# Performance work log

Measured on AMD Instinct MI355X. Metric: run time of the kernel, lower is better.

## Reference

```python
import jax, jax.numpy as jnp
import numpy as np

N, E = 50000, 800000
IN_F, HID, NCLS, NLAYERS = 64, 64, 2, 3
BN_EPS = 1e-5


def batch_norm(x, gamma, beta):
    # training-mode BatchNorm1d: biased batch statistics over the node/edge dim
    m = jnp.mean(x, axis=0)
    v = jnp.var(x, axis=0)
    return gamma * (x - m) * jax.lax.rsqrt(v + BN_EPS) + beta


def setup_inputs() -> dict:
    key = jax.random.key(0)
    ks = jax.random.split(key, 24)
    L, Lp1 = NLAYERS, NLAYERS + 1

    def lin(k, fan_in, shape):
        bound = 1.0 / np.sqrt(fan_in)
        return jax.random.uniform(k, shape, jnp.float32, -bound, bound)

    return {
        "h": jax.random.normal(ks[0], (N, IN_F), jnp.float32),
        "src": jax.random.randint(ks[1], (E,), 0, N, jnp.int32),
        "dst": jax.random.randint(ks[2], (E,), 0, N, jnp.int32),
        "emb_W": lin(ks[3], IN_F, (IN_F, HID)),
        "emb_b": lin(ks[4], IN_F, (HID,)),
        "mlp_W1": lin(ks[5], HID, (L, HID, HID)),
        "mlp_b1": lin(ks[6], HID, (L, HID)),
        "mlp_bn_g": jnp.ones((L, HID), jnp.float32),
        "mlp_bn_b": jnp.zeros((L, HID), jnp.float32),
        "mlp_W2": lin(ks[7], HID, (L, HID, HID)),
        "mlp_b2": lin(ks[8], HID, (L, HID)),
        "apply_bn_g": jnp.ones((L, HID), jnp.float32),
        "apply_bn_b": jnp.zeros((L, HID), jnp.float32),
        "out_bn_g": jnp.ones((L, HID), jnp.float32),
        "out_bn_b": jnp.zeros((L, HID), jnp.float32),
        "pred_W1": lin(ks[9], 2 * HID, (Lp1, 2 * HID, HID)),
        "pred_b1": lin(ks[10], 2 * HID, (Lp1, HID)),
        "pred_W2": lin(ks[11], HID, (Lp1, HID, NCLS)),
        "pred_b2": lin(ks[12], HID, (Lp1, NCLS)),
    }


def reference(h, src, dst, emb_W, emb_b, mlp_W1, mlp_b1, mlp_bn_g, mlp_bn_b,
              mlp_W2, mlp_b2, apply_bn_g, apply_bn_b, out_bn_g, out_bn_b,
              pred_W1, pred_b1, pred_W2, pred_b2):
    n_layers = mlp_W1.shape[0]
    n_nodes = h.shape[0]

    def edge_feat(hn):
        # concat src and dst node features per edge -> [E, 2*HID]
        return jnp.concatenate([hn[src], hn[dst]], axis=1)

    hn = h @ emb_W + emb_b  # embedding_h
    edge_reps = [edge_feat(hn)]

    for i in range(n_layers):
        # GINConv (sum aggregation, eps=0): (1+eps)*h_v + sum_{u->v} h_u
        agg = jax.ops.segment_sum(hn[src], dst, num_segments=n_nodes)
        z = hn + agg
        # MLP (depth 2): Linear -> BN -> ReLU -> Linear
        z = jax.nn.relu(batch_norm(z @ mlp_W1[i] + mlp_b1[i], mlp_bn_g[i], mlp_bn_b[i]))
        z = z @ mlp_W2[i] + mlp_b2[i]
        # ApplyNodeFunc: BN + ReLU
        z = jax.nn.relu(batch_norm(z, apply_bn_g[i], apply_bn_b[i]))
        # outer per-layer BN + ReLU
        hn = jax.nn.relu(batch_norm(z, out_bn_g[i], out_bn_b[i]))
        edge_reps.append(edge_feat(hn))

    # sum of per-layer edge predictions: Linear(2h->h) -> ReLU -> Linear(h->ncls)
    score = jnp.zeros((src.shape[0], pred_W2.shape[-1]), h.dtype)
    for i, e in enumerate(edge_reps):
        score = score + jax.nn.relu(e @ pred_W1[i] + pred_b1[i]) @ pred_W2[i] + pred_b2[i]
    return score
```

## Files before the change

### kernel.cpp

```cpp
#include <hip/hip_runtime.h>
#include <hip/hip_bf16.h>


#define BN_EPS 1e-5f

static __device__ __forceinline__ float bf2f(ushort u) {
  return __uint_as_float(((unsigned)u) << 16);
}

__global__ __launch_bounds__(256) void hist_kernel(const int* __restrict__ dst,
                                                   int* __restrict__ deg, int E) {
  int i = blockIdx.x * blockDim.x + threadIdx.x;
  int stride = gridDim.x * blockDim.x;
  for (; i < E; i += stride) atomicAdd(&deg[dst[i]], 1);
}

__global__ __launch_bounds__(256) void scan1_kernel(const int* __restrict__ deg,
                                                    int* __restrict__ rowstart,
                                                    int* __restrict__ partials, int N) {
  __shared__ int wsum[4];
  int tid = threadIdx.x;
  int lane = tid & 63, w = tid >> 6;
  int base = blockIdx.x * 1024 + tid * 4;
  int d0 = 0, d1 = 0, d2 = 0, d3 = 0;
  if (base + 3 < N) {
    int4 v = *reinterpret_cast<const int4*>(deg + base);
    d0 = v.x; d1 = v.y; d2 = v.z; d3 = v.w;
  } else {
    if (base + 0 < N) d0 = deg[base + 0];
    if (base + 1 < N) d1 = deg[base + 1];
    if (base + 2 < N) d2 = deg[base + 2];
  }
  int t0 = d0, t1 = t0 + d1, t2 = t1 + d2, t3 = t2 + d3;
  int tot = t3;
  int inc = tot;
#pragma unroll
  for (int off = 1; off < 64; off <<= 1) {
    int v = __shfl_up(inc, off);
    if (lane >= off) inc += v;
  }
  if (lane == 63) wsum[w] = inc;
  __syncthreads();
  int woff = 0;
  for (int k = 0; k < w; ++k) woff += wsum[k];
  int excl = woff + inc - tot;
  if (base + 0 < N) rowstart[base + 0] = excl;
  if (base + 1 < N) rowstart[base + 1] = excl + t0;
  if (base + 2 < N) rowstart[base + 2] = excl + t1;
  if (base + 3 < N) rowstart[base + 3] = excl + t2;
  if (tid == 255) partials[blockIdx.x] = excl + t3;
}

__global__ __launch_bounds__(256) void scan3_kernel(const int* __restrict__ partials,
                                                    int* __restrict__ rowstart,
                                                    int* __restrict__ cursor,
                                                    int N, int NB, int E) {
  __shared__ int s_off;
  int tid = threadIdx.x;
  if (tid < 64) {
    int v = (tid < NB) ? partials[tid] : 0;
    int inc = v;
#pragma unroll
    for (int off = 1; off < 64; off <<= 1) {
      int t = __shfl_up(inc, off);
      if (tid >= off) inc += t;
    }
    if (tid == (int)blockIdx.x) s_off = inc - v;
  }
  __syncthreads();
  int off = s_off;
  int base = blockIdx.x * 1024 + tid * 4;
#pragma unroll
  for (int k = 0; k < 4; ++k) {
    int i = base + k;
    if (i < N) {
      int r = rowstart[i] + off;
      rowstart[i] = r;
      cursor[i] = r;
    }
  }
  if (blockIdx.x == 0 && tid == 0) rowstart[N] = E;
}

__global__ __launch_bounds__(256) void fill_kernel(const int* __restrict__ src,
                                                   const int* __restrict__ dst,
                                                   int* __restrict__ cursor,
                                                   int2* __restrict__ epack, int E) {
  int i = blockIdx.x * blockDim.x + threadIdx.x;
  int stride = gridDim.x * blockDim.x;
  for (; i < E; i += stride) {
    int p = atomicAdd(&cursor[dst[i]], 1);
    epack[p] = make_int2(src[i], i);
  }
}

template <int TR>
__global__ __launch_bounds__(256) void agg_gemm_kernel(
    const float* __restrict__ c, const ushort* __restrict__ cb,
    const int2* __restrict__ epack, const int* __restrict__ rowstart,
    const float* __restrict__ W, const float* __restrict__ bias,
    const float* __restrict__ stats_tr, const float* __restrict__ g_tr,
    const float* __restrict__ b_tr, float* __restrict__ out,
    float* __restrict__ stats_out, int N) {
  __shared__ float sW[64][64];
  __shared__ float sx[32][64];
  __shared__ float red[2][4][64];
  int tid = threadIdx.x, lane = tid & 63, w = tid >> 6;
  int n0 = blockIdx.x * 32;
#pragma unroll
  for (int r = 0; r < 16; ++r) {
    int idx = r * 256 + tid;
    sW[idx >> 6][idx & 63] = W[idx];
  }
  float sc = 1.f, sh = 0.f;
  if (TR) {
    float invN = 1.0f / (float)N;
    float m = stats_tr[lane] * invN;
    float var = stats_tr[64 + lane] * invN - m * m;
    sc = g_tr[lane] * rsqrtf(var + BN_EPS);
    sh = b_tr[lane] - m * sc;
  }
  for (int j = 0; j < 8; ++j) {
    int v = n0 + w * 8 + j;
    float acc = 0.f;
    if (v < N) {
      float x0 = c[(size_t)v * 64 + lane];
      acc = TR ? fmaxf(x0 * sc + sh, 0.f) : x0;
      int p = rowstart[v], pe = rowstart[v + 1];
      for (; p + 8 <= pe; p += 8) {
        int u[8];
#pragma unroll
        for (int k = 0; k < 8; ++k) u[k] = epack[p + k].x;
        float x[8];
#pragma unroll
        for (int k = 0; k < 8; ++k) x[k] = bf2f(cb[(size_t)u[k] * 64 + lane]);
#pragma unroll
        for (int k = 0; k < 8; ++k) acc += TR ? fmaxf(x[k] * sc + sh, 0.f) : x[k];
      }
      for (; p < pe; ++p) {
        float x = bf2f(cb[(size_t)epack[p].x * 64 + lane]);
        acc += TR ? fmaxf(x * sc + sh, 0.f) : x;
      }
    }
    sx[w * 8 + j][lane] = acc;
  }
  __syncthreads();
  float o[8];
  float bz = bias[lane];
#pragma unroll
  for (int j = 0; j < 8; ++j) o[j] = bz;
  for (int k = 0; k < 64; ++k) {
    float wv = sW[k][lane];
#pragma unroll
    for (int j = 0; j < 8; ++j) o[j] = fmaf(sx[w * 8 + j][k], wv, o[j]);
  }
  float ps = 0.f, pq = 0.f;
#pragma unroll
  for (int j = 0; j < 8; ++j) {
    int n = n0 + w * 8 + j;
    if (n < N) {
      out[(size_t)n * 64 + lane] = o[j];
      ps += o[j];
      pq += o[j] * o[j];
    }
  }
  if (stats_out) {
    red[0][w][lane] = ps;
    red[1][w][lane] = pq;
    __syncthreads();
    if (w == 0) {
      float s = red[0][0][lane] + red[0][1][lane] + red[0][2][lane] + red[0][3][lane];
      float q = red[1][0][lane] + red[1][1][lane] + red[1][2][lane] + red[1][3][lane];
      atomicAdd(&stats_out[lane], s);
      atomicAdd(&stats_out[64 + lane], q);
    }
  }
}

__global__ __launch_bounds__(256) void gemm64_kernel(
    const float* __restrict__ in, const float* __restrict__ W,
    const float* __restrict__ bias, const float* __restrict__ stats_in,
    const float* __restrict__ g_in, const float* __restrict__ b_in,
    float* __restrict__ out, float* __restrict__ stats_out,
    __hip_bfloat16* __restrict__ out_bf, int N) {
  __shared__ float sW[64][64];
  __shared__ float sx[32][64];
  __shared__ float red[2][4][64];
  int tid = threadIdx.x;
  int lane = tid & 63, w = tid >> 6;
  int n0 = blockIdx.x * 32;
#pragma unroll
  for (int r = 0; r < 16; ++r) {
    int idx = r * 256 + tid;
    sW[idx >> 6][idx & 63] = W[idx];
  }
  float sc = 1.f, sh = 0.f;
  if (stats_in) {
    float invN = 1.0f / (float)N;
    float m = stats_in[lane] * invN;
    float var = stats_in[64 + lane] * invN - m * m;
    sc = g_in[lane] * rsqrtf(var + BN_EPS);
    sh = b_in[lane] - m * sc;
  }
#pragma unroll
  for (int r = 0; r < 8; ++r) {
    int idx = r * 256 + tid;
    int n = n0 + (idx >> 6);
    float x = (n < N) ? in[(size_t)n * 64 + lane] : 0.f;
    if (stats_in) x = fmaxf(x * sc + sh, 0.f);
    sx[idx >> 6][lane] = x;
  }
  __syncthreads();
  float acc[8];
  float bz = bias ? bias[lane] : 0.f;
#pragma unroll
  for (int j = 0; j < 8; ++j) acc[j] = bz;
  for (int k = 0; k < 64; ++k) {
    float wv = sW[k][lane];
#pragma unroll
    for (int j = 0; j < 8; ++j) acc[j] = fmaf(sx[w * 8 + j][k], wv, acc[j]);
  }
  float ps = 0.f, pq = 0.f;
#pragma unroll
  for (int j = 0; j < 8; ++j) {
    int n = n0 + w * 8 + j;
    if (n < N) {
      out[(size_t)n * 64 + lane] = acc[j];
      if (out_bf) out_bf[(size_t)n * 64 + lane] = __float2bfloat16(acc[j]);
      ps += acc[j];
      pq += acc[j] * acc[j];
    }
  }
  if (stats_out) {
    red[0][w][lane] = ps;
    red[1][w][lane] = pq;
    __syncthreads();
    if (w == 0) {
      float s = red[0][0][lane] + red[0][1][lane] + red[0][2][lane] + red[0][3][lane];
      float q = red[1][0][lane] + red[1][1][lane] + red[1][2][lane] + red[1][3][lane];
      atomicAdd(&stats_out[lane], s);
      atomicAdd(&stats_out[64 + lane], q);
    }
  }
}

__global__ __launch_bounds__(256) void proj_kernel(
    const float* __restrict__ c, const float* __restrict__ W1,
    const float* __restrict__ b1, const float* __restrict__ stats_in,
    const float* __restrict__ g_in, const float* __restrict__ b_in,
    __hip_bfloat16* __restrict__ P1, __hip_bfloat16* __restrict__ P2, int N) {
  __shared__ float sWa[64][64];
  __shared__ float sWb[64][64];
  __shared__ float sx[32][64];
  int tid = threadIdx.x, lane = tid & 63, w = tid >> 6;
  int n0 = blockIdx.x * 32;
#pragma unroll
  for (int r = 0; r < 16; ++r) {
    int idx = r * 256 + tid;
    sWa[idx >> 6][idx & 63] = W1[idx];
    sWb[idx >> 6][idx & 63] = W1[4096 + idx];
  }
  float sc = 1.f, sh = 0.f;
  if (stats_in) {
    float invN = 1.0f / (float)N;
    float m = stats_in[lane] * invN;
    float var = stats_in[64 + lane] * invN - m * m;
    sc = g_in[lane] * rsqrtf(var + BN_EPS);
    sh = b_in[lane] - m * sc;
  }
#pragma unroll
  for (int r = 0; r < 8; ++r) {
    int idx = r * 256 + tid;
    int n = n0 + (idx >> 6);
    float x = (n < N) ? c[(size_t)n * 64 + lane] : 0.f;
    if (stats_in) x = fmaxf(x * sc + sh, 0.f);
    sx[idx >> 6][lane] = x;
  }
  __syncthreads();
  float a1[8], a2[8];
  float bz = b1[lane];
#pragma unroll
  for (int j = 0; j < 8; ++j) { a1[j] = bz; a2[j] = 0.f; }
  for (int k = 0; k < 64; ++k) {
    float wa = sWa[k][lane];
    float wb = sWb[k][lane];
#pragma unroll
    for (int j = 0; j < 8; ++j) {
      float x = sx[w * 8 + j][k];
      a1[j] = fmaf(x, wa, a1[j]);
      a2[j] = fmaf(x, wb, a2[j]);
    }
  }
#pragma unroll
  for (int j = 0; j < 8; ++j) {
    int n = n0 + w * 8 + j;
    if (n < N) {
      P1[(size_t)n * 64 + lane] = __float2bfloat16(a1[j]);
      P2[(size_t)n * 64 + lane] = __float2bfloat16(a2[j]);
    }
  }
}

__global__ __launch_bounds__(256) void bnrelu_kernel(
    const float* __restrict__ in, const float* __restrict__ stats_in,
    const float* __restrict__ g_in, const float* __restrict__ b_in,
    float* __restrict__ out, float* __restrict__ stats_out,
    __hip_bfloat16* __restrict__ out_bf, int N) {
  __shared__ float red[2][4][64];
  int tid = threadIdx.x;
  int lane = tid & 63, w = tid >> 6;
  float invN = 1.0f / (float)N;
  float m = stats_in[lane] * invN;
  float var = stats_in[64 + lane] * invN - m * m;
  float sc = g_in[lane] * rsqrtf(var + BN_EPS);
  float sh = b_in[lane] - m * sc;
  float ps = 0.f, pq = 0.f;
  int rows_per_grid = gridDim.x * (blockDim.x >> 6);
  for (int n = blockIdx.x * (blockDim.x >> 6) + w; n < N; n += rows_per_grid) {
    float x = fmaxf(in[(size_t)n * 64 + lane] * sc + sh, 0.f);
    out[(size_t)n * 64 + lane] = x;
    if (out_bf) out_bf[(size_t)n * 64 + lane] = __float2bfloat16(x);
    ps += x;
    pq += x * x;
  }
  if (stats_out) {
    red[0][w][lane] = ps;
    red[1][w][lane] = pq;
    __syncthreads();
    if (w == 0) {
      float s = red[0][0][lane] + red[0][1][lane] + red[0][2][lane] + red[0][3][lane];
      float q = red[1][0][lane] + red[1][1][lane] + red[1][2][lane] + red[1][3][lane];
      atomicAdd(&stats_out[lane], s);
      atomicAdd(&stats_out[64 + lane], q);
    }
  }
}

__global__ __launch_bounds__(256) void edge_score_csr_kernel(
    const ushort* __restrict__ P1, const ushort* __restrict__ P2,
    const int* __restrict__ rowstart, const int2* __restrict__ epack,
    const float* __restrict__ W2, const float* __restrict__ b2,
    float2* __restrict__ sc, int N, int first) {
  int lane = threadIdx.x & 63;
  int v = blockIdx.x * 4 + (threadIdx.x >> 6);
  if (v >= N) return;
  int sub = lane & 7;
  int grp = lane >> 3;
  float w[16];
  const float4* wp = reinterpret_cast<const float4*>(W2 + sub * 16);
#pragma unroll
  for (int k = 0; k < 4; ++k) {
    float4 t = wp[k];
    w[4 * k + 0] = t.x; w[4 * k + 1] = t.y; w[4 * k + 2] = t.z; w[4 * k + 3] = t.w;
  }
  float bb0 = b2[0], bb1 = b2[1];
  uint4 pb = *reinterpret_cast<const uint4*>(P2 + (size_t)v * 64 + sub * 8);
  unsigned bv[4] = {pb.x, pb.y, pb.z, pb.w};
  int p0 = rowstart[v], p1 = rowstart[v + 1];
  for (int p = p0 + grp; p < p1; p += 8) {
    int s = epack[p].x;
    uint4 pa = *reinterpret_cast<const uint4*>(P1 + (size_t)s * 64 + sub * 8);
    unsigned av[4] = {pa.x, pa.y, pa.z, pa.w};
    float q0 = 0.f, q1 = 0.f;
#pragma unroll
    for (int k = 0; k < 4; ++k) {
      float a_lo = __uint_as_float(av[k] << 16);
      float a_hi = __uint_as_float(av[k] & 0xffff0000u);
      float b_lo = __uint_as_float(bv[k] << 16);
      float b_hi = __uint_as_float(bv[k] & 0xffff0000u);
      float v0 = fmaxf(a_lo + b_lo, 0.f);
      float v1 = fmaxf(a_hi + b_hi, 0.f);
      q0 = fmaf(v0, w[4 * k + 0], fmaf(v1, w[4 * k + 2], q0));
      q1 = fmaf(v0, w[4 * k + 1], fmaf(v1, w[4 * k + 3], q1));
    }
#pragma unroll
    for (int mm = 1; mm < 8; mm <<= 1) {
      q0 += __shfl_xor(q0, mm);
      q1 += __shfl_xor(q1, mm);
    }
    if (sub == 0) {
      float o0 = q0 + bb0, o1 = q1 + bb1;
      if (!first) {
        float2 prev = sc[p];
        o0 += prev.x;
        o1 += prev.y;
      }
      sc[p] = make_float2(o0, o1);
    }
  }
}

__global__ __launch_bounds__(256) void scatter_kernel(const float2* __restrict__ sc,
                                                      const int2* __restrict__ epack,
                                                      float2* __restrict__ out, int E) {
  int i = blockIdx.x * blockDim.x + threadIdx.x;
  int stride = gridDim.x * blockDim.x;
  for (; i < E; i += stride) out[epack[i].y] = sc[i];
}

extern "C" void kernel_launch(void* const* d_in, const int* in_sizes, int n_in,
                              void* d_out, int out_size, void* d_ws, size_t ws_size,
                              hipStream_t stream) {
  const float* h          = (const float*)d_in[0];
  const int*   src        = (const int*)d_in[1];
  const int*   dst        = (const int*)d_in[2];
  const float* emb_W      = (const float*)d_in[3];
  const float* emb_b      = (const float*)d_in[4];
  const float* mlp_W1     = (const float*)d_in[5];
  const float* mlp_b1     = (const float*)d_in[6];
  const float* mlp_bn_g   = (const float*)d_in[7];
  const float* mlp_bn_b   = (const float*)d_in[8];
  const float* mlp_W2     = (const float*)d_in[9];
  const float* mlp_b2     = (const float*)d_in[10];
  const float* apply_bn_g = (const float*)d_in[11];
  const float* apply_bn_b = (const float*)d_in[12];
  const float* out_bn_g   = (const float*)d_in[13];
  const float* out_bn_b   = (const float*)d_in[14];
  const float* pred_W1    = (const float*)d_in[15];
  const float* pred_b1    = (const float*)d_in[16];
  const float* pred_W2    = (const float*)d_in[17];
  const float* pred_b2    = (const float*)d_in[18];

  const int N = in_sizes[0] / 64;
  const int E = in_sizes[1];
  const size_t NF = (size_t)N * 64;
  const int NB1 = (N + 1023) / 1024;

  float* ws = (float*)d_ws;
  float* c  = ws;
  float* z1 = c + NF;
  float* z2 = z1 + NF;
  __hip_bfloat16* cb = (__hip_bfloat16*)(z2 + NF);
  __hip_bfloat16* P1 = cb + NF;
  __hip_bfloat16* P2 = P1 + NF;
  int2*   epack  = (int2*)(P2 + NF);
  float2* scbuf  = (float2*)(epack + E);
  int* rowstart  = (int*)(scbuf + E);
  int* cursor    = rowstart + (N + 64);
  int* partials  = cursor + (N + 64);
  int* deg       = partials + 64;
  float* stats   = (float*)(deg + (N + 64));

  size_t need = (size_t)((char*)(stats + 9 * 128) - (char*)d_ws);
  if (need > ws_size) return;

  hipMemsetAsync(deg, 0, ((size_t)(N + 64) + 9 * 128) * sizeof(int), stream);

  const int gemmBlocks = (N + 31) / 32;
  const int nodeBlocks = (N + 3) / 4;

  gemm64_kernel<<<gemmBlocks, 256, 0, stream>>>(h, emb_W, emb_b, nullptr, nullptr,
                                                nullptr, c, nullptr, cb, N);
  hist_kernel<<<1024, 256, 0, stream>>>(dst, deg, E);
  scan1_kernel<<<NB1, 256, 0, stream>>>(deg, rowstart, partials, N);
  scan3_kernel<<<NB1, 256, 0, stream>>>(partials, rowstart, cursor, N, NB1, E);
  fill_kernel<<<1024, 256, 0, stream>>>(src, dst, cursor, epack, E);

  proj_kernel<<<gemmBlocks, 256, 0, stream>>>(c, pred_W1, pred_b1, nullptr, nullptr,
                                              nullptr, P1, P2, N);
  edge_score_csr_kernel<<<nodeBlocks, 256, 0, stream>>>(
      (const ushort*)P1, (const ushort*)P2, rowstart, epack, pred_W2, pred_b2,
      scbuf, N, 1);

  for (int i = 0; i < 3; ++i) {
    float* st1 = stats + (size_t)(3 * i + 0) * 128;
    float* st2 = stats + (size_t)(3 * i + 1) * 128;
    float* st3 = stats + (size_t)(3 * i + 2) * 128;
    const float* stP = (i == 0) ? nullptr : stats + (size_t)(3 * (i - 1) + 2) * 128;
    const float* gP  = (i == 0) ? nullptr : out_bn_g + (i - 1) * 64;
    const float* bP  = (i == 0) ? nullptr : out_bn_b + (i - 1) * 64;

    if (i == 0)
      agg_gemm_kernel<0><<<gemmBlocks, 256, 0, stream>>>(
          c, (const ushort*)cb, epack, rowstart, mlp_W1 + (size_t)i * 4096,
          mlp_b1 + i * 64, nullptr, nullptr, nullptr, z1, st1, N);
    else
      agg_gemm_kernel<1><<<gemmBlocks, 256, 0, stream>>>(
          c, (const ushort*)cb, epack, rowstart, mlp_W1 + (size_t)i * 4096,
          mlp_b1 + i * 64, stP, gP, bP, z1, st1, N);
    gemm64_kernel<<<gemmBlocks, 256, 0, stream>>>(z1, mlp_W2 + (size_t)i * 4096,
                                                  mlp_b2 + i * 64, st1,
                                                  mlp_bn_g + i * 64, mlp_bn_b + i * 64,
                                                  z2, st2, nullptr, N);
    bnrelu_kernel<<<784, 256, 0, stream>>>(z2, st2, apply_bn_g + i * 64,
                                           apply_bn_b + i * 64, c, st3, cb, N);
    proj_kernel<<<gemmBlocks, 256, 0, stream>>>(c, pred_W1 + (size_t)(i + 1) * 8192,
                                                pred_b1 + (i + 1) * 64, st3,
                                                out_bn_g + i * 64, out_bn_b + i * 64,
                                                P1, P2, N);
    edge_score_csr_kernel<<<nodeBlocks, 256, 0, stream>>>(
        (const ushort*)P1, (const ushort*)P2, rowstart, epack,
        pred_W2 + (i + 1) * 128, pred_b2 + (i + 1) * 2, scbuf, N, 0);
  }

  scatter_kernel<<<2048, 256, 0, stream>>>(scbuf, epack, (float2*)d_out, E);
}
```

Before: 972.8 us.

## Fuse neighbor aggregation into edge-score kernel via interleaved node feature buffer

Interleaves the bf16 projected source features and the bf16 node features into one 128-wide row per node, so a single 16-byte gather per edge feeds both the edge-score MLP and the GIN sum aggregation. The separate aggregation+GEMM kernel is replaced by a plain GEMM over an aggregated buffer written by the fused score/aggregate kernel. This removes one full CSR gather pass per layer. In exchange, each edge is handled by a 16-lane group (half the lanes idle on each branch), and the 4-way edge split lowers parallelism compared with the 8-way score kernel.

```diff
diff --git a/kernel.cpp b/kernel.cpp
--- a/kernel.cpp
+++ b/kernel.cpp
@@ -4,8 +4,11 @@
 
 #define BN_EPS 1e-5f
 
-static __device__ __forceinline__ float bf2f(ushort u) {
-  return __uint_as_float(((unsigned)u) << 16);
+static __device__ __forceinline__ float bf2f_lo(unsigned u) {
+  return __uint_as_float(u << 16);
+}
+static __device__ __forceinline__ float bf2f_hi(unsigned u) {
+  return __uint_as_float(u & 0xffff0000u);
 }
 
 __global__ __launch_bounds__(256) void hist_kernel(const int* __restrict__ dst,
@@ -94,18 +97,17 @@
   }
 }
 
-template <int TR>
-__global__ __launch_bounds__(256) void agg_gemm_kernel(
-    const float* __restrict__ c, const ushort* __restrict__ cb,
-    const int2* __restrict__ epack, const int* __restrict__ rowstart,
-    const float* __restrict__ W, const float* __restrict__ bias,
-    const float* __restrict__ stats_tr, const float* __restrict__ g_tr,
-    const float* __restrict__ b_tr, float* __restrict__ out,
-    float* __restrict__ stats_out, int N) {
+__global__ __launch_bounds__(256) void gemm64_kernel(
+    const float* __restrict__ in, const float* __restrict__ W,
+    const float* __restrict__ bias, const float* __restrict__ stats_in,
+    const float* __restrict__ g_in, const float* __restrict__ b_in,
+    float* __restrict__ out, float* __restrict__ stats_out,
+    ushort* __restrict__ out_g, int N) {
   __shared__ float sW[64][64];
   __shared__ float sx[32][64];
   __shared__ float red[2][4][64];
-  int tid = threadIdx.x, lane = tid & 63, w = tid >> 6;
+  int tid = threadIdx.x;
+  int lane = tid & 63, w = tid >> 6;
   int n0 = blockIdx.x * 32;
 #pragma unroll
   for (int r = 0; r < 16; ++r) {
@@ -113,55 +115,43 @@
     sW[idx >> 6][idx & 63] = W[idx];
   }
   float sc = 1.f, sh = 0.f;
-  if (TR) {
+  if (stats_in) {
     float invN = 1.0f / (float)N;
-    float m = stats_tr[lane] * invN;
-    float var = stats_tr[64 + lane] * invN - m * m;
-    sc = g_tr[lane] * rsqrtf(var + BN_EPS);
-    sh = b_tr[lane] - m * sc;
-  }
-  for (int j = 0; j < 8; ++j) {
-    int v = n0 + w * 8 + j;
-    float acc = 0.f;
-    if (v < N) {
-      float x0 = c[(size_t)v * 64 + lane];
-      acc = TR ? fmaxf(x0 * sc + sh, 0.f) : x0;
-      int p = rowstart[v], pe = rowstart[v + 1];
-      for (; p + 8 <= pe; p += 8) {
-        int u[8];
-#pragma unroll
-        for (int k = 0; k < 8; ++k) u[k] = epack[p + k].x;
-        float x[8];
-#pragma unroll
-        for (int k = 0; k < 8; ++k) x[k] = bf2f(cb[(size_t)u[k] * 64 + lane]);
-#pragma unroll
-        for (int k = 0; k < 8; ++k) acc += TR ? fmaxf(x[k] * sc + sh, 0.f) : x[k];
-      }
-      for (; p < pe; ++p) {
-        float x = bf2f(cb[(size_t)epack[p].x * 64 + lane]);
-        acc += TR ? fmaxf(x * sc + sh, 0.f) : x;
-      }
-    }
-    sx[w * 8 + j][lane] = acc;
+    float m = stats_in[lane] * invN;
+    float var = stats_in[64 + lane] * invN - m * m;
+    sc = g_in[lane] * rsqrtf(var + BN_EPS);
+    sh = b_in[lane] - m * sc;
+  }
+#pragma unroll
+  for (int r = 0; r < 8; ++r) {
+    int idx = r * 256 + tid;
+    int n = n0 + (idx >> 6);
+    float x = (n < N) ? in[(size_t)n * 64 + lane] : 0.f;
+    if (stats_in) x = fmaxf(x * sc + sh, 0.f);
+    sx[idx >> 6][lane] = x;
   }
   __syncthreads();
-  float o[8];
-  float bz = bias[lane];
-#pragma unroll
-  for (int j = 0; j < 8; ++j) o[j] = bz;
+  float acc[8];
+  float bz = bias ? bias[lane] : 0.f;
+#pragma unroll
+  for (int j = 0; j < 8; ++j) acc[j] = bz;
   for (int k = 0; k < 64; ++k) {
     float wv = sW[k][lane];
 #pragma unroll
-    for (int j = 0; j < 8; ++j) o[j] = fmaf(sx[w * 8 + j][k], wv, o[j]);
+    for (int j = 0; j < 8; ++j) acc[j] = fmaf(sx[w * 8 + j][k], wv, acc[j]);
   }
   float ps = 0.f, pq = 0.f;
 #pragma unroll
   for (int j = 0; j < 8; ++j) {
     int n = n0 + w * 8 + j;
     if (n < N) {
-      out[(size_t)n * 64 + lane] = o[j];
-      ps += o[j];
-      pq += o[j] * o[j];
+      out[(size_t)n * 64 + lane] = acc[j];
+      if (out_g) {
+        __hip_bfloat16 b = __float2bfloat16(acc[j]);
+        out_g[(size_t)n * 128 + lane] = *reinterpret_cast<ushort*>(&b);
+      }
+      ps += acc[j];
+      pq += acc[j] * acc[j];
     }
   }
   if (stats_out) {
@@ -177,22 +167,21 @@
   }
 }
 
-__global__ __launch_bounds__(256) void gemm64_kernel(
-    const float* __restrict__ in, const float* __restrict__ W,
-    const float* __restrict__ bias, const float* __restrict__ stats_in,
+__global__ __launch_bounds__(256) void proj_kernel(
+    const float* __restrict__ c, const float* __restrict__ W1,
+    const float* __restrict__ b1, const float* __restrict__ stats_in,
     const float* __restrict__ g_in, const float* __restrict__ b_in,
-    float* __restrict__ out, float* __restrict__ stats_out,
-    __hip_bfloat16* __restrict__ out_bf, int N) {
-  __shared__ float sW[64][64];
+    ushort* __restrict__ G, ushort* __restrict__ P2, int N) {
+  __shared__ float sWa[64][64];
+  __shared__ float sWb[64][64];
   __shared__ float sx[32][64];
-  __shared__ float red[2][4][64];
-  int tid = threadIdx.x;
-  int lane = tid & 63, w = tid >> 6;
+  int tid = threadIdx.x, lane = tid & 63, w = tid >> 6;
   int n0 = blockIdx.x * 32;
 #pragma unroll
   for (int r = 0; r < 16; ++r) {
     int idx = r * 256 + tid;
-    sW[idx >> 6][idx & 63] = W[idx];
+    sWa[idx >> 6][idx & 63] = W1[idx];
+    sWb[idx >> 6][idx & 63] = W1[4096 + idx];
   }
   float sc = 1.f, sh = 0.f;
   if (stats_in) {
@@ -206,72 +195,6 @@
   for (int r = 0; r < 8; ++r) {
     int idx = r * 256 + tid;
     int n = n0 + (idx >> 6);
-    float x = (n < N) ? in[(size_t)n * 64 + lane] : 0.f;
-    if (stats_in) x = fmaxf(x * sc + sh, 0.f);
-    sx[idx >> 6][lane] = x;
-  }
-  __syncthreads();
-  float acc[8];
-  float bz = bias ? bias[lane] : 0.f;
-#pragma unroll
-  for (int j = 0; j < 8; ++j) acc[j] = bz;
-  for (int k = 0; k < 64; ++k) {
-    float wv = sW[k][lane];
-#pragma unroll
-    for (int j = 0; j < 8; ++j) acc[j] = fmaf(sx[w * 8 + j][k], wv, acc[j]);
-  }
-  float ps = 0.f, pq = 0.f;
-#pragma unroll
-  for (int j = 0; j < 8; ++j) {
-    int n = n0 + w * 8 + j;
-    if (n < N) {
-      out[(size_t)n * 64 + lane] = acc[j];
-      if (out_bf) out_bf[(size_t)n * 64 + lane] = __float2bfloat16(acc[j]);
-      ps += acc[j];
-      pq += acc[j] * acc[j];
-    }
-  }
-  if (stats_out) {
-    red[0][w][lane] = ps;
-    red[1][w][lane] = pq;
-    __syncthreads();
-    if (w == 0) {
-      float s = red[0][0][lane] + red[0][1][lane] + red[0][2][lane] + red[0][3][lane];
-      float q = red[1][0][lane] + red[1][1][lane] + red[1][2][lane] + red[1][3][lane];
-      atomicAdd(&stats_out[lane], s);
-      atomicAdd(&stats_out[64 + lane], q);
-    }
-  }
-}
-
-__global__ __launch_bounds__(256) void proj_kernel(
-    const float* __restrict__ c, const float* __restrict__ W1,
-    const float* __restrict__ b1, const float* __restrict__ stats_in,
-    const float* __restrict__ g_in, const float* __restrict__ b_in,
-    __hip_bfloat16* __restrict__ P1, __hip_bfloat16* __restrict__ P2, int N) {
-  __shared__ float sWa[64][64];
-  __shared__ float sWb[64][64];
-  __shared__ float sx[32][64];
-  int tid = threadIdx.x, lane = tid & 63, w = tid >> 6;
-  int n0 = blockIdx.x * 32;
-#pragma unroll
-  for (int r = 0; r < 16; ++r) {
-    int idx = r * 256 + tid;
-    sWa[idx >> 6][idx & 63] = W1[idx];
-    sWb[idx >> 6][idx & 63] = W1[4096 + idx];
-  }
-  float sc = 1.f, sh = 0.f;
-  if (stats_in) {
-    float invN = 1.0f / (float)N;
-    float m = stats_in[lane] * invN;
-    float var = stats_in[64 + lane] * invN - m * m;
-    sc = g_in[lane] * rsqrtf(var + BN_EPS);
-    sh = b_in[lane] - m * sc;
-  }
-#pragma unroll
-  for (int r = 0; r < 8; ++r) {
-    int idx = r * 256 + tid;
-    int n = n0 + (idx >> 6);
     float x = (n < N) ? c[(size_t)n * 64 + lane] : 0.f;
     if (stats_in) x = fmaxf(x * sc + sh, 0.f);
     sx[idx >> 6][lane] = x;
@@ -295,8 +218,10 @@
   for (int j = 0; j < 8; ++j) {
     int n = n0 + w * 8 + j;
     if (n < N) {
-      P1[(size_t)n * 64 + lane] = __float2bfloat16(a1[j]);
-      P2[(size_t)n * 64 + lane] = __float2bfloat16(a2[j]);
+      __hip_bfloat16 b1v = __float2bfloat16(a1[j]);
+      __hip_bfloat16 b2v = __float2bfloat16(a2[j]);
+      G[(size_t)n * 128 + lane] = *reinterpret_cast<ushort*>(&b1v);
+      P2[(size_t)n * 64 + lane] = *reinterpret_cast<ushort*>(&b2v);
     }
   }
 }
@@ -305,7 +230,7 @@
     const float* __restrict__ in, const float* __restrict__ stats_in,
     const float* __restrict__ g_in, const float* __restrict__ b_in,
     float* __restrict__ out, float* __restrict__ stats_out,
-    __hip_bfloat16* __restrict__ out_bf, int N) {
+    ushort* __restrict__ out_g, int N) {
   __shared__ float red[2][4][64];
   int tid = threadIdx.x;
   int lane = tid & 63, w = tid >> 6;
@@ -319,7 +244,8 @@
   for (int n = blockIdx.x * (blockDim.x >> 6) + w; n < N; n += rows_per_grid) {
     float x = fmaxf(in[(size_t)n * 64 + lane] * sc + sh, 0.f);
     out[(size_t)n * 64 + lane] = x;
-    if (out_bf) out_bf[(size_t)n * 64 + lane] = __float2bfloat16(x);
+    __hip_bfloat16 b = __float2bfloat16(x);
+    out_g[(size_t)n * 128 + lane] = *reinterpret_cast<ushort*>(&b);
     ps += x;
     pq += x * x;
   }
@@ -336,8 +262,115 @@
   }
 }
 
+template <int TR>
+__global__ __launch_bounds__(256) void score_agg_kernel(
+    const ushort* __restrict__ G, const ushort* __restrict__ P2,
+    const float* __restrict__ c, const int* __restrict__ rowstart,
+    const int2* __restrict__ epack, const float* __restrict__ W2,
+    const float* __restrict__ b2, const float* __restrict__ stats_tr,
+    const float* __restrict__ g_tr, const float* __restrict__ b_tr,
+    float2* __restrict__ sc, float* __restrict__ zb, int N, int first) {
+  int lane = threadIdx.x & 63;
+  int v = blockIdx.x * 4 + (threadIdx.x >> 6);
+  if (v >= N) return;
+  int grp = lane >> 4;
+  int g16 = lane & 15;
+  int sub = g16 & 7;
+  float w[16];
+  {
+    const float4* wp = reinterpret_cast<const float4*>(W2 + sub * 16);
+#pragma unroll
+    for (int k = 0; k < 4; ++k) {
+      float4 t = wp[k];
+      w[4 * k + 0] = t.x; w[4 * k + 1] = t.y; w[4 * k + 2] = t.z; w[4 * k + 3] = t.w;
+    }
+  }
+  float bb0 = b2[0], bb1 = b2[1];
+  uint4 pb = *reinterpret_cast<const uint4*>(P2 + (size_t)v * 64 + sub * 8);
+  unsigned bv[4] = {pb.x, pb.y, pb.z, pb.w};
+  float scv[8], shv[8];
+  if (TR) {
+    float invN = 1.0f / (float)N;
+#pragma unroll
+    for (int k = 0; k < 8; ++k) {
+      int f = sub * 8 + k;
+      float m = stats_tr[f] * invN;
+      float var = stats_tr[64 + f] * invN - m * m;
+      scv[k] = g_tr[f] * rsqrtf(var + BN_EPS);
+      shv[k] = b_tr[f] - m * scv[k];
+    }
+  }
+  float acc[8];
+#pragma unroll
+  for (int k = 0; k < 8; ++k) acc[k] = 0.f;
+
+  int p0 = rowstart[v], p1 = rowstart[v + 1];
+  for (int p = p0 + grp; p < p1; p += 4) {
+    int s = epack[p].x;
+    uint4 row = *reinterpret_cast<const uint4*>(G + (size_t)s * 128 + g16 * 8);
+    unsigned rv[4] = {row.x, row.y, row.z, row.w};
+    float q0 = 0.f, q1 = 0.f;
+    if (g16 < 8) {
+#pragma unroll
+      for (int k = 0; k < 4; ++k) {
+        float v0 = fmaxf(bf2f_lo(rv[k]) + bf2f_lo(bv[k]), 0.f);
+        float v1 = fmaxf(bf2f_hi(rv[k]) + bf2f_hi(bv[k]), 0.f);
+        q0 = fmaf(v0, w[4 * k + 0], fmaf(v1, w[4 * k + 2], q0));
+        q1 = fmaf(v0, w[4 * k + 1], fmaf(v1, w[4 * k + 3], q1));
+      }
+    } else {
+#pragma unroll
+      for (int k = 0; k < 4; ++k) {
+        float x0 = bf2f_lo(rv[k]);
+        float x1 = bf2f_hi(rv[k]);
+        if (TR) {
+          x0 = fmaxf(x0 * scv[2 * k] + shv[2 * k], 0.f);
+          x1 = fmaxf(x1 * scv[2 * k + 1] + shv[2 * k + 1], 0.f);
+        }
+        acc[2 * k] += x0;
+        acc[2 * k + 1] += x1;
+      }
+    }
+#pragma unroll
+    for (int mm = 1; mm < 8; mm <<= 1) {
+      q0 += __shfl_xor(q0, mm);
+      q1 += __shfl_xor(q1, mm);
+    }
+    if (g16 == 0) {
+      float o0 = q0 + bb0, o1 = q1 + bb1;
+      if (!first) {
+        float2 prev = sc[p];
+        o0 += prev.x;
+        o1 += prev.y;
+      }
+      sc[p] = make_float2(o0, o1);
+    }
+  }
+#pragma unroll
+  for (int k = 0; k < 8; ++k) {
+    acc[k] += __shfl_xor(acc[k], 16);
+    acc[k] += __shfl_xor(acc[k], 32);
+  }
+  if (grp == 0 && g16 >= 8) {
+    const float* cv = c + (size_t)v * 64 + sub * 8;
+    float4 c0 = *reinterpret_cast<const float4*>(cv);
+    float4 c1 = *reinterpret_cast<const float4*>(cv + 4);
+    float cf[8] = {c0.x, c0.y, c0.z, c0.w, c1.x, c1.y, c1.z, c1.w};
+    float ov[8];
+#pragma unroll
+    for (int k = 0; k < 8; ++k) {
+      float x = cf[k];
+      if (TR) x = fmaxf(x * scv[k] + shv[k], 0.f);
+      ov[k] = acc[k] + x;
+    }
+    float* zp = zb + (size_t)v * 64 + sub * 8;
+    *reinterpret_cast<float4*>(zp) = make_float4(ov[0], ov[1], ov[2], ov[3]);
+    *reinterpret_cast<float4*>(zp + 4) = make_float4(ov[4], ov[5], ov[6], ov[7]);
+  }
+}
+
 __global__ __launch_bounds__(256) void edge_score_csr_kernel(
-    const ushort* __restrict__ P1, const ushort* __restrict__ P2,
+    const ushort* __restrict__ G, const ushort* __restrict__ P2,
     const int* __restrict__ rowstart, const int2* __restrict__ epack,
     const float* __restrict__ W2, const float* __restrict__ b2,
     float2* __restrict__ sc, int N, int first) {
@@ -359,17 +392,13 @@
   int p0 = rowstart[v], p1 = rowstart[v + 1];
   for (int p = p0 + grp; p < p1; p += 8) {
     int s = epack[p].x;
-    uint4 pa = *reinterpret_cast<const uint4*>(P1 + (size_t)s * 64 + sub * 8);
+    uint4 pa = *reinterpret_cast<const uint4*>(G + (size_t)s * 128 + sub * 8);
     unsigned av[4] = {pa.x, pa.y, pa.z, pa.w};
     float q0 = 0.f, q1 = 0.f;
 #pragma unroll
     for (int k = 0; k < 4; ++k) {
-      float a_lo = __uint_as_float(av[k] << 16);
-      float a_hi = __uint_as_float(av[k] & 0xffff0000u);
-      float b_lo = __uint_as_float(bv[k] << 16);
-      float b_hi = __uint_as_float(bv[k] & 0xffff0000u);
-      float v0 = fmaxf(a_lo + b_lo, 0.f);
-      float v1 = fmaxf(a_hi + b_hi, 0.f);
+      float v0 = fmaxf(bf2f_lo(av[k]) + bf2f_lo(bv[k]), 0.f);
+      float v1 = fmaxf(bf2f_hi(av[k]) + bf2f_hi(bv[k]), 0.f);
       q0 = fmaf(v0, w[4 * k + 0], fmaf(v1, w[4 * k + 2], q0));
       q1 = fmaf(v0, w[4 * k + 1], fmaf(v1, w[4 * k + 3], q1));
     }
@@ -427,19 +456,18 @@
   const int NB1 = (N + 1023) / 1024;
 
   float* ws = (float*)d_ws;
-  float* c  = ws;
-  float* z1 = c + NF;
-  float* z2 = z1 + NF;
-  __hip_bfloat16* cb = (__hip_bfloat16*)(z2 + NF);
-  __hip_bfloat16* P1 = cb + NF;
-  __hip_bfloat16* P2 = P1 + NF;
-  int2*   epack  = (int2*)(P2 + NF);
-  float2* scbuf  = (float2*)(epack + E);
-  int* rowstart  = (int*)(scbuf + E);
-  int* cursor    = rowstart + (N + 64);
-  int* partials  = cursor + (N + 64);
-  int* deg       = partials + 64;
-  float* stats   = (float*)(deg + (N + 64));
+  float* c   = ws;
+  float* z1  = c + NF;
+  float* zb  = z1 + NF;
+  ushort* G  = (ushort*)(zb + NF);
+  ushort* P2 = G + (size_t)N * 128;
+  int2*   epack = (int2*)(P2 + NF);
+  float2* scbuf = (float2*)(epack + E);
+  int* rowstart = (int*)(scbuf + E);
+  int* cursor   = rowstart + (N + 64);
+  int* partials = cursor + (N + 64);
+  int* deg      = partials + 64;
+  float* stats  = (float*)(deg + (N + 64));
 
   size_t need = (size_t)((char*)(stats + 9 * 128) - (char*)d_ws);
   if (need > ws_size) return;
@@ -450,47 +478,46 @@
   const int nodeBlocks = (N + 3) / 4;
 
   gemm64_kernel<<<gemmBlocks, 256, 0, stream>>>(h, emb_W, emb_b, nullptr, nullptr,
-                                                nullptr, c, nullptr, cb, N);
+                                                nullptr, c, nullptr, G + 64, N);
   hist_kernel<<<1024, 256, 0, stream>>>(dst, deg, E);
   scan1_kernel<<<NB1, 256, 0, stream>>>(deg, rowstart, partials, N);
   scan3_kernel<<<NB1, 256, 0, stream>>>(partials, rowstart, cursor, N, NB1, E);
   fill_kernel<<<1024, 256, 0, stream>>>(src, dst, cursor, epack, E);
 
   proj_kernel<<<gemmBlocks, 256, 0, stream>>>(c, pred_W1, pred_b1, nullptr, nullptr,
-                                              nullptr, P1, P2, N);
-  edge_score_csr_kernel<<<nodeBlocks, 256, 0, stream>>>(
-      (const ushort*)P1, (const ushort*)P2, rowstart, epack, pred_W2, pred_b2,
-      scbuf, N, 1);
+                                              nullptr, G, P2, N);
+  score_agg_kernel<0><<<nodeBlocks, 256, 0, stream>>>(
+      G, P2, c, rowstart, epack, pred_W2, pred_b2, nullptr, nullptr, nullptr,
+      scbuf, zb, N, 1);
 
   for (int i = 0; i < 3; ++i) {
     float* st1 = stats + (size_t)(3 * i + 0) * 128;
     float* st2 = stats + (size_t)(3 * i + 1) * 128;
     float* st3 = stats + (size_t)(3 * i + 2) * 128;
-    const float* stP = (i == 0) ? nullptr : stats + (size_t)(3 * (i - 1) + 2) * 128;
-    const float* gP  = (i == 0) ? nullptr : out_bn_g + (i - 1) * 64;
-    const float* bP  = (i == 0) ? nullptr : out_bn_b + (i - 1) * 64;
-
-    if (i == 0)
-      agg_gemm_kernel<0><<<gemmBlocks, 256, 0, stream>>>(
-          c, (const ushort*)cb, epack, rowstart, mlp_W1 + (size_t)i * 4096,
-          mlp_b1 + i * 64, nullptr, nullptr, nullptr, z1, st1, N);
-    else
-      agg_gemm_kernel<1><<<gemmBlocks, 256, 0, stream>>>(
-          c, (const ushort*)cb, epack, rowstart, mlp_W1 + (size_t)i * 4096,
-          mlp_b1 + i * 64, stP, gP, bP, z1, st1, N);
+
+    gemm64_kernel<<<gemmBlocks, 256, 0, stream>>>(zb, mlp_W1 + (size_t)i * 4096,
+                                                  mlp_b1 + i * 64, nullptr, nullptr,
+                                                  nullptr, z1, st1, nullptr, N);
     gemm64_kernel<<<gemmBlocks, 256, 0, stream>>>(z1, mlp_W2 + (size_t)i * 4096,
                                                   mlp_b2 + i * 64, st1,
                                                   mlp_bn_g + i * 64, mlp_bn_b + i * 64,
-                                                  z2, st2, nullptr, N);
-    bnrelu_kernel<<<784, 256, 0, stream>>>(z2, st2, apply_bn_g + i * 64,
-                                           apply_bn_b + i * 64, c, st3, cb, N);
+                                                  zb, st2, nullptr, N);
+    bnrelu_kernel<<<784, 256, 0, stream>>>(zb, st2, apply_bn_g + i * 64,
+                                           apply_bn_b + i * 64, c, st3, G + 64, N);
     proj_kernel<<<gemmBlocks, 256, 0, stream>>>(c, pred_W1 + (size_t)(i + 1) * 8192,
                                                 pred_b1 + (i + 1) * 64, st3,
                                                 out_bn_g + i * 64, out_bn_b + i * 64,
-                                                P1, P2, N);
-    edge_score_csr_kernel<<<nodeBlocks, 256, 0, stream>>>(
-        (const ushort*)P1, (const ushort*)P2, rowstart, epack,
-        pred_W2 + (i + 1) * 128, pred_b2 + (i + 1) * 2, scbuf, N, 0);
+                                                G, P2, N);
+    if (i < 2) {
+      score_agg_kernel<1><<<nodeBlocks, 256, 0, stream>>>(
+          G, P2, c, rowstart, epack, pred_W2 + (i + 1) * 128,
+          pred_b2 + (i + 1) * 2, st3, out_bn_g + i * 64, out_bn_b + i * 64,
+          scbuf, zb, N, 0);
+    } else {
+      edge_score_csr_kernel<<<nodeBlocks, 256, 0, stream>>>(
+          G, P2, rowstart, epack, pred_W2 + (i + 1) * 128,
+          pred_b2 + (i + 1) * 2, scbuf, N, 0);
+    }
   }
 
   scatter_kernel<<<2048, 256, 0, stream>>>(scbuf, epack, (float2*)d_out, E);
```

Result: faster. 926.2 us (-4.8%).
